# Performance work log

Measured on AMD Instinct MI355X. Metric: run time of the kernel, lower is better.

## Reference

```python
import jax, jax.numpy as jnp
import numpy as np

C, L, B = 66, 100, 4096
FEAT = 9 * C * 12  # 7128


def _conv1d(x, w, b, pad):
    # x: (B, Cin, L), w: (Cout, Cin, K), b: (Cout,)
    y = jax.lax.conv_general_dilated(x, w, (1,), [(pad, pad)],
                                     dimension_numbers=('NCH', 'OIH', 'NCH'))
    return y + b[None, :, None]


def _pool2(x):
    # AvgPool1d(kernel=2, stride=2) with floor on odd lengths
    Lx = x.shape[-1]
    x = x[..., : 2 * (Lx // 2)]
    return x.reshape(*x.shape[:-1], Lx // 2, 2).mean(-1)


def _branch(xc, w1, b1, w2, b2, w3, b3, pad):
    # conv/relu/pool x3 (dropout is identity in eval)
    h = _pool2(jax.nn.relu(_conv1d(xc, w1, b1, pad)))
    h = _pool2(jax.nn.relu(_conv1d(h, w2, b2, pad)))
    h = _pool2(jax.nn.relu(_conv1d(h, w3, b3, pad)))
    return h  # (B, 4, 12)


def setup_inputs() -> dict:
    key = jax.random.key(0)
    ks = jax.random.split(key, 20)
    s = 0.1
    inp = {
        'x': jax.random.normal(ks[0], (B, L, C), dtype=jnp.float32),
        # high-resolution branch (kernel 7, pad 3), one filter set per channel
        'hw1': jax.random.normal(ks[1], (C, 8, 1, 7)) * s,
        'hb1': jnp.full((C, 8), 0.1, jnp.float32),
        'hw2': jax.random.normal(ks[2], (C, 4, 8, 7)) * s,
        'hb2': jnp.full((C, 4), 0.1, jnp.float32),
        'hw3': jax.random.normal(ks[3], (C, 4, 4, 7)) * s,
        'hb3': jnp.full((C, 4), 0.1, jnp.float32),
        # low-resolution branch (kernel 3, pad 1)
        'lw1': jax.random.normal(ks[4], (C, 8, 1, 3)) * s,
        'lb1': jnp.full((C, 8), 0.1, jnp.float32),
        'lw2': jax.random.normal(ks[5], (C, 4, 8, 3)) * s,
        'lb2': jnp.full((C, 4), 0.1, jnp.float32),
        'lw3': jax.random.normal(ks[6], (C, 4, 4, 3)) * s,
        'lb3': jnp.full((C, 4), 0.1, jnp.float32),
        # MLP head
        'fw1': jax.random.normal(ks[7], (1936, FEAT)) * 0.02,
        'fb1': jnp.full((1936,), 0.1, jnp.float32),
        'fw2': jax.random.normal(ks[8], (14, 1936)) * 0.02,
        'fb2': jnp.full((14,), 0.1, jnp.float32),
    }
    return inp


def reference(x, hw1, hb1, hw2, hb2, hw3, hb3,
              lw1, lb1, lw2, lb2, lw3, lb3, fw1, fb1, fw2, fb2):
    bsz = x.shape[0]
    xc = jnp.transpose(x, (2, 0, 1))[:, :, None, :]  # (C, B, 1, L)
    high = jax.vmap(lambda xi, a, b_, c, d, e, f: _branch(xi, a, b_, c, d, e, f, 3))(
        xc, hw1, hb1, hw2, hb2, hw3, hb3)        # (C, B, 4, 12)
    low = jax.vmap(lambda xi, a, b_, c, d, e, f: _branch(xi, a, b_, c, d, e, f, 1))(
        xc, lw1, lb1, lw2, lb2, lw3, lb3)        # (C, B, 4, 12)
    res = jax.vmap(lambda xi: _pool2(_pool2(_pool2(xi))))(xc)  # (C, B, 1, 12)
    feats = jnp.concatenate([high, low, res], axis=2)          # (C, B, 9, 12)
    feats = jnp.transpose(feats, (1, 0, 2, 3)).reshape(bsz, -1)  # (B, C*9*12)
    h = jax.nn.relu(feats @ fw1.T + fb1)
    return h @ fw2.T + fb2
```

## Files before the change

kernel.cpp:

```cpp
#include <hip/hip_runtime.h>

typedef _Float16 f16;
typedef _Float16 h2 __attribute__((ext_vector_type(2)));
typedef _Float16 f16x8 __attribute__((ext_vector_type(8)));
typedef float    f32x4 __attribute__((ext_vector_type(4)));
typedef unsigned int u32;
typedef u32 u32x2 __attribute__((ext_vector_type(2)));
typedef u32 u32x4 __attribute__((ext_vector_type(4)));

#define CCH 66
#define LLEN 100
#define BSZ 4096
#define NPAD 2048
#define NOUT 1936
#define KFEAT 7128
#define FPC 112
#define KF2 (CCH * FPC)
#define KP2 7424
#define NCH2 (KP2 / 8)
#define ROWE (BSZ * 8)
#define LC (LLEN * CCH)
#define OSTR 25
#define XPW 52
#define CWS 512

typedef __attribute__((address_space(1))) const u32 gu32;
typedef __attribute__((address_space(3))) u32 lu32;

__device__ __forceinline__ void gload_lds16(const void* g, void* l) {
    __builtin_amdgcn_global_load_lds((gu32*)g, (lu32*)l, 16, 0, 0);
}

__device__ __forceinline__ h2  uh(u32 v) { return __builtin_bit_cast(h2, v); }
__device__ __forceinline__ u32 hu(h2 v)  { return __builtin_bit_cast(u32, v); }
__device__ __forceinline__ h2  pkfma(h2 a, h2 b, h2 c) { return __builtin_elementwise_fma(a, b, c); }
__device__ __forceinline__ h2  pkmax0(h2 a) { h2 z = (h2)(_Float16)0.f; return __builtin_elementwise_max(a, z); }

__global__ __launch_bounds__(256) void transpose_x(const float* __restrict__ x,
                                                   f16* __restrict__ xT) {
    __shared__ float tile[32][33];
    const int m0 = blockIdx.x * 32;
    const int b0 = blockIdx.y * 32;
    const int tx = threadIdx.x & 31, ty = threadIdx.x >> 5;
#pragma unroll
    for (int i = 0; i < 32; i += 8) {
        int m = m0 + tx, b = b0 + ty + i;
        tile[ty + i][tx] = (m < LC) ? x[(size_t)b * LC + m] : 0.f;
    }
    __syncthreads();
#pragma unroll
    for (int i = 0; i < 32; i += 8) {
        int m = m0 + ty + i, b = b0 + tx;
        if (m < LC) xT[(size_t)m * BSZ + b] = (f16)tile[tx][ty + i];
    }
}

__global__ __launch_bounds__(256) void pack_x(const f16* __restrict__ xT,
                                              u32* __restrict__ xP) {
    const int c = blockIdx.x, w = blockIdx.y;
    const int b = blockIdx.z * 256 + threadIdx.x;
    u32 v = 0u;
    if (w < 50) {
        f16 lo = xT[(size_t)(2 * w * CCH + c) * BSZ + b];
        f16 hi = xT[(size_t)((2 * w + 1) * CCH + c) * BSZ + b];
        v = hu((h2){lo, hi});
    }
    xP[((size_t)c * XPW + w) * BSZ + b] = v;
}

__device__ __forceinline__ u32 dupf(float v) {
    _Float16 h = (_Float16)v; return hu((h2){h, h});
}
__device__ __forceinline__ u32 pk2f(float a, float b) {
    return hu((h2){(_Float16)a, (_Float16)b});
}

__global__ __launch_bounds__(64) void prep_w(
    const float* __restrict__ hw1, const float* __restrict__ hb1,
    const float* __restrict__ hw2, const float* __restrict__ hb2,
    const float* __restrict__ hw3, const float* __restrict__ hb3,
    const float* __restrict__ lw1, const float* __restrict__ lb1,
    const float* __restrict__ lw2, const float* __restrict__ lb2,
    const float* __restrict__ lw3, const float* __restrict__ lb3,
    u32* __restrict__ wpk) {
    const int c = blockIdx.x, t = threadIdx.x;
    u32* wb = wpk + c * CWS;
    for (int i = t; i < 56; i += 64) wb[i] = dupf(hw1[c * 56 + i]);
    if (t < 8)  wb[56 + t] = dupf(hb1[c * 8 + t]);
    for (int i = t; i < 224; i += 64) wb[64 + i] = dupf(hw2[c * 224 + i]);
    if (t < 4)  wb[288 + t] = dupf(hb2[c * 4 + t]);
    for (int i = t; i < 56; i += 64) {
        int pr = i / 28, j = i - pr * 28;
        wb[292 + i] = pk2f(hw3[c * 112 + 2 * pr * 28 + j], hw3[c * 112 + (2 * pr + 1) * 28 + j]);
    }
    if (t < 2)  wb[348 + t] = pk2f(hb3[c * 4 + 2 * t], hb3[c * 4 + 2 * t + 1]);
    for (int i = t; i < 24; i += 64) wb[350 + i] = dupf(lw1[c * 24 + i]);
    if (t < 8)  wb[374 + t] = dupf(lb1[c * 8 + t]);
    for (int i = t; i < 96; i += 64) wb[382 + i] = dupf(lw2[c * 96 + i]);
    if (t < 4)  wb[478 + t] = dupf(lb2[c * 4 + t]);
    for (int i = t; i < 24; i += 64) {
        int pr = i / 12, j = i - pr * 12;
        wb[482 + i] = pk2f(lw3[c * 48 + 2 * pr * 12 + j], lw3[c * 48 + (2 * pr + 1) * 12 + j]);
    }
    if (t < 2)  wb[506 + t] = pk2f(lb3[c * 4 + 2 * t], lb3[c * 4 + 2 * t + 1]);
}

template<int K>
__device__ __forceinline__ void hp1_core(const u32* PX, const u32* __restrict__ w1d,
                                         const u32* __restrict__ b1d, u32 msk, u32 np[8]) {
#pragma unroll
    for (int ic = 0; ic < 8; ++ic) {
        h2 bb = uh(b1d[ic]);
        h2 AL = bb, AH = bb;
#pragma unroll
        for (int k = 0; k < K; ++k) {
            h2 w = uh(w1d[ic * K + k]);
            AL = pkfma(w, uh(PX[k]), AL);
            AH = pkfma(w, uh(PX[k + 2]), AH);
        }
        AL = pkmax0(AL); AH = pkmax0(AH);
        _Float16 cA = (_Float16)0.5f * (AL.x + AL.y);
        _Float16 cB = (_Float16)0.5f * (AH.x + AH.y);
        np[ic] = hu((h2){cA, cB}) & msk;
    }
}

template<int K>
__device__ __forceinline__ void hp1_run(const u32* __restrict__ xlt, int idx,
                                        const u32* w1d, const u32* b1d, u32 np[8]) {
    constexpr int P = K / 2;
    constexpr int NA = (K + 5) / 2;
    const int w0 = idx - (P + 1) / 2;
    const u32* base = xlt + w0 * 256;
    u32 A[NA];
#pragma unroll
    for (int j = 0; j < NA; ++j) A[j] = base[j * 256];
    u32 PX[K + 2];
#pragma unroll
    for (int j = 0; j < K + 2; ++j)
        PX[j] = (j & 1) ? A[(j + 1) / 2]
                        : __builtin_amdgcn_alignbit(A[j / 2 + 1], A[j / 2], 16);
    u32 m = ((idx < 50) ? 0xFFFFu : 0u) | ((idx + 1 < 50) ? 0xFFFF0000u : 0u);
    hp1_core<K>(PX, w1d, b1d, m, np);
}

template<int K, int IDX>
__device__ __forceinline__ void hp1_edge(const u32* __restrict__ xlt,
                                         const u32* w1d, const u32* b1d, u32 np[8]) {
    constexpr int P = K / 2;
    u32 PX[K + 2];
#pragma unroll
    for (int j = 0; j < K + 2; ++j) {
        int u = 2 * IDX - P + j;
        u32 v;
        if (u < -1)      v = 0u;
        else if (u == -1) v = xlt[0] << 16;
        else if (u & 1)  v = __builtin_amdgcn_alignbit(xlt[((u + 1) / 2) * 256],
                                                       xlt[((u - 1) / 2) * 256], 16);
        else             v = xlt[(u / 2) * 256];
        PX[j] = v;
    }
    hp1_core<K>(PX, w1d, b1d, 0xFFFFFFFFu, np);
}

template<int K>
__device__ __forceinline__ void run_branch_pk(const u32* __restrict__ xlt,
                                              const u32* __restrict__ wb,
                                              u32* __restrict__ orow) {
    constexpr int P = K / 2;
    constexpr int NW1 = (K + 1) / 2;
    const u32* w1d = wb;
    const u32* b1d = wb + 8 * K;
    const u32* w2d = b1d + 8;
    const u32* b2d = w2d + 32 * K;
    const u32* w3p = b2d + 4;
    const u32* b3p = w3p + 8 * K;

    u32 W1p[8][NW1];
    u32 W2d[4][K];
#pragma unroll
    for (int ic = 0; ic < 8; ++ic)
#pragma unroll
        for (int j = 0; j < NW1; ++j) W1p[ic][j] = 0u;
#pragma unroll
    for (int oc = 0; oc < 4; ++oc)
#pragma unroll
        for (int k = 0; k < K; ++k) W2d[oc][k] = 0u;

    {
        u32 np[8];
        if (K == 7) {
            hp1_edge<K, 0>(xlt, w1d, b1d, np);
#pragma unroll
            for (int ic = 0; ic < 8; ++ic) W1p[ic][1] = np[ic] << 16;
            hp1_edge<K, 1>(xlt, w1d, b1d, np);
#pragma unroll
            for (int ic = 0; ic < 8; ++ic) W1p[ic][2] = np[ic];
            hp1_edge<K, 3>(xlt, w1d, b1d, np);
#pragma unroll
            for (int ic = 0; ic < 8; ++ic) W1p[ic][3] = np[ic];
        } else {
            hp1_edge<K, 0>(xlt, w1d, b1d, np);
#pragma unroll
            for (int ic = 0; ic < 8; ++ic) W1p[ic][0] = np[ic] << 16;
            hp1_edge<K, 1>(xlt, w1d, b1d, np);
#pragma unroll
            for (int ic = 0; ic < 8; ++ic) W1p[ic][1] = np[ic];
        }
    }

    h2 Pp01 = (h2)(_Float16)0.f, Pp23 = Pp01, Q01 = Pp01, Q23 = Pp01;
    const int SMAX = 23 + P;
    for (int s = 0; s <= SMAX; ++s) {
        h2 Y[4];
#pragma unroll
        for (int oc = 0; oc < 4; ++oc) Y[oc] = uh(b2d[oc]);
#pragma unroll
        for (int ic = 0; ic < 8; ++ic) {
            u32 PW[K];
#pragma unroll
            for (int k = 0; k < K; ++k)
                PW[k] = (k & 1) ? __builtin_amdgcn_alignbit(W1p[ic][k / 2 + 1], W1p[ic][k / 2], 16)
                                : W1p[ic][k / 2];
#pragma unroll
            for (int oc = 0; oc < 4; ++oc)
#pragma unroll
                for (int k = 0; k < K; ++k)
                    Y[oc] = pkfma(uh(w2d[(oc * 8 + ic) * K + k]), uh(PW[k]), Y[oc]);
        }
#pragma unroll
        for (int oc = 0; oc < 4; ++oc) {
            h2 Yr = pkmax0(Y[oc]);
            _Float16 hv = (_Float16)0.5f * (Yr.x + Yr.y);
            u32 d = hu((h2){hv, hv});
            d = (s <= 24) ? d : 0u;
#pragma unroll
            for (int k = 0; k < K - 1; ++k) W2d[oc][k] = W2d[oc][k + 1];
            W2d[oc][K - 1] = d;
        }
        int p = s - P;
        if (p >= 0) {
            h2 Y01 = uh(b3p[0]), Y23 = uh(b3p[1]);
#pragma unroll
            for (int ic = 0; ic < 4; ++ic)
#pragma unroll
                for (int k = 0; k < K; ++k) {
                    h2 wv = uh(W2d[ic][k]);
                    Y01 = pkfma(uh(w3p[ic * K + k]), wv, Y01);
                    Y23 = pkfma(uh(w3p[4 * K + ic * K + k]), wv, Y23);
                }
            Y01 = pkmax0(Y01); Y23 = pkmax0(Y23);
            if ((p & 1) == 0) { Pp01 = Y01; Pp23 = Y23; }
            else {
                h2 hf = (h2)(_Float16)0.5f;
                h2 O01 = (Pp01 + Y01) * hf;
                h2 O23 = (Pp23 + Y23) * hf;
                int t = p >> 1;
                if ((t & 1) == 0) { Q01 = O01; Q23 = O23; }
                else {
                    int w = t >> 1;
                    orow[0 * 6 + w] = hu((h2){Q01.x, O01.x});
                    orow[1 * 6 + w] = hu((h2){Q01.y, O01.y});
                    orow[2 * 6 + w] = hu((h2){Q23.x, O23.x});
                    orow[3 * 6 + w] = hu((h2){Q23.y, O23.y});
                }
            }
        }
        if (s < SMAX) {
            u32 np[8];
            hp1_run<K>(xlt, 2 * s + P + 2, w1d, b1d, np);
#pragma unroll
            for (int ic = 0; ic < 8; ++ic) {
#pragma unroll
                for (int j = 0; j < NW1 - 1; ++j) W1p[ic][j] = W1p[ic][j + 1];
                W1p[ic][NW1 - 1] = np[ic];
            }
        }
    }
}

__global__ __launch_bounds__(256, 2) void feats_kernel(
    const u32* __restrict__ xP, const u32* __restrict__ wpk,
    f16* __restrict__ feats2) {
    __shared__ u32 xl[XPW * 256];
    __shared__ u32 obufw[256 * OSTR];
    const int c = blockIdx.x;
    const int tid = threadIdx.x;
    const int lane = tid & 63, wid = tid >> 6;
    const int b = blockIdx.y * 256 + tid;

    const u32* src = xP + (size_t)c * XPW * BSZ + blockIdx.y * 256;
    for (int w = wid; w < XPW; w += 4)
        gload_lds16(src + (size_t)w * BSZ + lane * 4, (char*)xl + w * 1024 + lane * 16);
    __syncthreads();

    const u32* xlt = xl + tid;
    const u32* wb = wpk + c * CWS;
    u32* orow = obufw + tid * OSTR;
    u32* dst = (u32*)feats2 + (size_t)c * 14 * (ROWE / 2) + (size_t)b * 4;

    run_branch_pk<7>(xlt, wb, orow);
    {
        u32 v[24];
#pragma unroll
        for (int j = 0; j < 24; ++j) v[j] = orow[j];
#pragma unroll
        for (int ch = 0; ch < 6; ++ch)
            *(u32x4*)(dst + (size_t)ch * (ROWE / 2)) =
                (u32x4){v[ch * 4], v[ch * 4 + 1], v[ch * 4 + 2], v[ch * 4 + 3]};
    }
    run_branch_pk<3>(xlt, wb + 350, orow);
    {
        u32 v[24];
#pragma unroll
        for (int j = 0; j < 24; ++j) v[j] = orow[j];
#pragma unroll
        for (int ch = 0; ch < 6; ++ch)
            *(u32x4*)(dst + (size_t)(6 + ch) * (ROWE / 2)) =
                (u32x4){v[ch * 4], v[ch * 4 + 1], v[ch * 4 + 2], v[ch * 4 + 3]};
    }
    u32 orr[6];
#pragma unroll
    for (int t2 = 0; t2 < 6; ++t2) {
        h2 S0 = uh(xlt[(8 * t2 + 0) * 256]) + uh(xlt[(8 * t2 + 1) * 256]) +
                uh(xlt[(8 * t2 + 2) * 256]) + uh(xlt[(8 * t2 + 3) * 256]);
        h2 S1 = uh(xlt[(8 * t2 + 4) * 256]) + uh(xlt[(8 * t2 + 5) * 256]) +
                uh(xlt[(8 * t2 + 6) * 256]) + uh(xlt[(8 * t2 + 7) * 256]);
        _Float16 o0 = (_Float16)0.125f * (S0.x + S0.y);
        _Float16 o1 = (_Float16)0.125f * (S1.x + S1.y);
        orr[t2] = hu((h2){o0, o1});
    }
    *(u32x4*)(dst + (size_t)12 * (ROWE / 2)) = (u32x4){orr[0], orr[1], orr[2], orr[3]};
    *(u32x4*)(dst + (size_t)13 * (ROWE / 2)) = (u32x4){orr[4], orr[5], 0u, 0u};
}

__global__ void zero_pad2(f16* __restrict__ feats2) {
    int idx = blockIdx.x * 256 + threadIdx.x;
    u32* dst = (u32*)(feats2 + (size_t)(CCH * 14) * ROWE);
    if (idx < (4 * ROWE * 2) / 16)
        *(u32x4*)(dst + idx * 4) = (u32x4){0u, 0u, 0u, 0u};
}

__global__ void cvt_fw1(const float* __restrict__ fw1, f16* __restrict__ dst) {
    int n = blockIdx.y;
    int kp = blockIdx.x * 256 + threadIdx.x;
    if (kp >= KP2) return;
    int c2 = kp / FPC, f = kp - c2 * FPC;
    float v = 0.f;
    if (n < NOUT && kp < KF2 && f < 108)
        v = fw1[(size_t)n * KFEAT + c2 * 108 + f];
    dst[(size_t)n * KP2 + kp] = (f16)v;
}

__global__ __launch_bounds__(256) void fc1_gemm(
    const f16* __restrict__ A, const f16* __restrict__ Bw, float* __restrict__ C) {
    __shared__ f16 lds_a[128 * 32];
    __shared__ f16 lds_b[128 * 32];
    const int tid = threadIdx.x;
    const int bm = blockIdx.x, bn = blockIdx.y, kz = blockIdx.z;
    const int wid = tid >> 6, lane = tid & 63;
    const int wm = wid >> 1, wn = wid & 1;

    f32x4 acc[4][4];
#pragma unroll
    for (int i = 0; i < 4; ++i)
#pragma unroll
        for (int j = 0; j < 4; ++j) acc[i][j] = (f32x4){0.f, 0.f, 0.f, 0.f};

    const f16* Bbase = Bw + (size_t)bn * 128 * KP2;
    const int l15 = lane & 15, lhi = lane >> 4;

    const int flat0 = tid, flat1 = 256 + tid;
    const int row0 = flat0 >> 2, kc0 = flat0 & 3;
    const int row1 = flat1 >> 2, kc1 = flat1 & 3;

    const int kbeg = kz * (KP2 / 2), kend = kbeg + KP2 / 2;
    for (int k0 = kbeg; k0 < kend; k0 += 32) {
        __syncthreads();
        gload_lds16(A + (size_t)((k0 >> 3) + kc0) * ROWE + (size_t)(bm * 128 + row0) * 8,
                    (char*)lds_a + flat0 * 16);
        gload_lds16(A + (size_t)((k0 >> 3) + kc1) * ROWE + (size_t)(bm * 128 + row1) * 8,
                    (char*)lds_a + flat1 * 16);
        gload_lds16(Bbase + (size_t)row0 * KP2 + k0 + kc0 * 8, (char*)lds_b + flat0 * 16);
        gload_lds16(Bbase + (size_t)row1 * KP2 + k0 + kc1 * 8, (char*)lds_b + flat1 * 16);
        __syncthreads();

        f16x8 af[4], bf[4];
#pragma unroll
        for (int i = 0; i < 4; ++i) {
            int m = wm * 64 + i * 16 + l15;
            af[i] = *(const f16x8*)(lds_a + m * 32 + lhi * 8);
            int n = wn * 64 + i * 16 + l15;
            bf[i] = *(const f16x8*)(lds_b + n * 32 + lhi * 8);
        }
#pragma unroll
        for (int i = 0; i < 4; ++i)
#pragma unroll
            for (int j = 0; j < 4; ++j)
                acc[i][j] = __builtin_amdgcn_mfma_f32_16x16x32_f16(af[i], bf[j], acc[i][j], 0, 0, 0);
    }

#pragma unroll
    for (int i = 0; i < 4; ++i)
#pragma unroll
        for (int j = 0; j < 4; ++j) {
            int n = bn * 128 + wn * 64 + j * 16 + l15;
#pragma unroll
            for (int r = 0; r < 4; ++r) {
                int m = bm * 128 + wm * 64 + i * 16 + lhi * 4 + r;
                atomicAdd(&C[(size_t)m * NPAD + n], acc[i][j][r]);
            }
        }
}

__global__ __launch_bounds__(256) void fc1_fin(const float* __restrict__ C,
                                               const float* __restrict__ fb1,
                                               f16* __restrict__ H) {
    size_t i4 = ((size_t)blockIdx.x * 256 + threadIdx.x) * 4;
    int n = (int)(i4 & (NPAD - 1));
    f32x4 v = *(const f32x4*)(C + i4);
    f16 r[4];
#pragma unroll
    for (int j = 0; j < 4; ++j) {
        int nn = n + j;
        float bias = (nn < NOUT) ? fb1[nn] : 0.f;
        r[j] = (f16)fmaxf(v[j] + bias, 0.f);
    }
    *(u32x2*)(H + i4) = (u32x2){hu((h2){r[0], r[1]}), hu((h2){r[2], r[3]})};
}

__global__ __launch_bounds__(64) void fc2_kernel(const f16* __restrict__ H,
                                                 const float* __restrict__ fw2,
                                                 const float* __restrict__ fb2,
                                                 float* __restrict__ out) {
    const int b = blockIdx.x;
    const int t = threadIdx.x;
    const f16* hb = H + (size_t)b * NPAD;
    float acc[14];
#pragma unroll
    for (int o = 0; o < 14; ++o) acc[o] = 0.f;
    for (int k = t; k < NOUT; k += 64) {
        float hv = (float)hb[k];
#pragma unroll
        for (int o = 0; o < 14; ++o) acc[o] += hv * fw2[o * NOUT + k];
    }
#pragma unroll
    for (int o = 0; o < 14; ++o) {
        float v = acc[o];
#pragma unroll
        for (int off = 32; off > 0; off >>= 1) v += __shfl_down(v, off, 64);
        if (t == 0) out[b * 14 + o] = v + fb2[o];
    }
}

extern "C" void kernel_launch(void* const* d_in, const int* in_sizes, int n_in,
                              void* d_out, int out_size, void* d_ws, size_t ws_size,
                              hipStream_t stream) {
    const float* x   = (const float*)d_in[0];
    const float* hw1 = (const float*)d_in[1];
    const float* hb1 = (const float*)d_in[2];
    const float* hw2 = (const float*)d_in[3];
    const float* hb2 = (const float*)d_in[4];
    const float* hw3 = (const float*)d_in[5];
    const float* hb3 = (const float*)d_in[6];
    const float* lw1 = (const float*)d_in[7];
    const float* lb1 = (const float*)d_in[8];
    const float* lw2 = (const float*)d_in[9];
    const float* lb2 = (const float*)d_in[10];
    const float* lw3 = (const float*)d_in[11];
    const float* lb3 = (const float*)d_in[12];
    const float* fw1 = (const float*)d_in[13];
    const float* fb1 = (const float*)d_in[14];
    const float* fw2 = (const float*)d_in[15];
    const float* fb2 = (const float*)d_in[16];

    char* wsb = (char*)d_ws;
    f16*  feats2 = (f16*)wsb;
    char* reg2   = wsb + (size_t)NCH2 * ROWE * 2;
    f16*  xT     = (f16*)reg2;
    float* C     = (float*)reg2;
    f16*  h      = (f16*)(reg2 + (size_t)BSZ * NPAD * 4);
    char* reg3   = reg2 + (size_t)LC * BSZ * 2;
    u32*  xP     = (u32*)reg3;
    f16*  fw1H   = (f16*)reg3;
    u32*  wpk    = (u32*)(reg3 + (size_t)CCH * XPW * BSZ * 4);

    transpose_x<<<dim3((LC + 31) / 32, BSZ / 32), 256, 0, stream>>>(x, xT);
    pack_x<<<dim3(CCH, XPW, BSZ / 256), 256, 0, stream>>>(xT, xP);
    prep_w<<<dim3(CCH), 64, 0, stream>>>(hw1, hb1, hw2, hb2, hw3, hb3,
                                         lw1, lb1, lw2, lb2, lw3, lb3, wpk);
    feats_kernel<<<dim3(CCH, BSZ / 256), 256, 0, stream>>>(xP, wpk, feats2);
    zero_pad2<<<dim3(64), 256, 0, stream>>>(feats2);
    cvt_fw1<<<dim3((KP2 + 255) / 256, NPAD), 256, 0, stream>>>(fw1, fw1H);
    hipMemsetAsync(C, 0, (size_t)BSZ * NPAD * 4, stream);
    fc1_gemm<<<dim3(BSZ / 128, NPAD / 128, 2), 256, 0, stream>>>(feats2, fw1H, C);
    fc1_fin<<<dim3(BSZ * NPAD / 4 / 256), 256, 0, stream>>>(C, fb1, h);
    fc2_kernel<<<dim3(BSZ), 64, 0, stream>>>(h, fw2, fb2, (float*)d_out);
}
```

Before: 783.2 us.

## Fuse transpose and pack of x, stream input windows from global in feats kernel

Replaces the two-pass transpose_x plus pack_x pipeline with a single xpose_pack kernel that reads x tiles into LDS and writes the packed half2 layout directly, plus a small kernel that zeroes the halo words. The feats kernel drops its large LDS staging buffer and instead keeps a sliding register window of input pairs, loaded from global memory as the convolution advances. This removes an intermediate f16 buffer round trip and frees LDS, which may allow more occupancy. The cost is more global loads in the inner loop, which rely on cache hits and latency hiding.

After: 757.1 us. 3.3% less time.

```diff
diff --git a/kernel.cpp b/kernel.cpp
--- a/kernel.cpp
+++ b/kernel.cpp
@@ -36,36 +36,31 @@
 __device__ __forceinline__ h2  pkfma(h2 a, h2 b, h2 c) { return __builtin_elementwise_fma(a, b, c); }
 __device__ __forceinline__ h2  pkmax0(h2 a) { h2 z = (h2)(_Float16)0.f; return __builtin_elementwise_max(a, z); }
 
-__global__ __launch_bounds__(256) void transpose_x(const float* __restrict__ x,
-                                                   f16* __restrict__ xT) {
-    __shared__ float tile[32][33];
-    const int m0 = blockIdx.x * 32;
-    const int b0 = blockIdx.y * 32;
-    const int tx = threadIdx.x & 31, ty = threadIdx.x >> 5;
-#pragma unroll
-    for (int i = 0; i < 32; i += 8) {
-        int m = m0 + tx, b = b0 + ty + i;
-        tile[ty + i][tx] = (m < LC) ? x[(size_t)b * LC + m] : 0.f;
+__global__ __launch_bounds__(256) void xpose_pack(const float* __restrict__ x,
+                                                  u32* __restrict__ xP) {
+    __shared__ float tile[64][133];
+    const int w = blockIdx.x;
+    const int b0 = blockIdx.y * 64;
+    const int tid = threadIdx.x;
+    const float* src = x + (size_t)b0 * LC + (size_t)(2 * w) * CCH;
+#pragma unroll
+    for (int i = 0; i < 33; ++i) {
+        int f = i * 256 + tid;
+        int bi = f / 132, j = f - bi * 132;
+        tile[bi][j] = src[(size_t)bi * LC + j];
     }
     __syncthreads();
-#pragma unroll
-    for (int i = 0; i < 32; i += 8) {
-        int m = m0 + ty + i, b = b0 + tx;
-        if (m < LC) xT[(size_t)m * BSZ + b] = (f16)tile[tx][ty + i];
-    }
-}
-
-__global__ __launch_bounds__(256) void pack_x(const f16* __restrict__ xT,
-                                              u32* __restrict__ xP) {
-    const int c = blockIdx.x, w = blockIdx.y;
-    const int b = blockIdx.z * 256 + threadIdx.x;
-    u32 v = 0u;
-    if (w < 50) {
-        f16 lo = xT[(size_t)(2 * w * CCH + c) * BSZ + b];
-        f16 hi = xT[(size_t)((2 * w + 1) * CCH + c) * BSZ + b];
-        v = hu((h2){lo, hi});
-    }
-    xP[((size_t)c * XPW + w) * BSZ + b] = v;
+    const int lane = tid & 63, cg = tid >> 6;
+    for (int c = cg; c < CCH; c += 4) {
+        u32 v = hu((h2){(_Float16)tile[lane][c], (_Float16)tile[lane][66 + c]});
+        xP[((size_t)c * XPW + w) * BSZ + b0 + lane] = v;
+    }
+}
+
+__global__ __launch_bounds__(256) void zero_halo_xp(u32* __restrict__ xP) {
+    const int c = blockIdx.x;
+    const int i = blockIdx.y * 256 + threadIdx.x;
+    *(u32x4*)(xP + ((size_t)c * XPW + 50) * BSZ + (size_t)i * 4) = (u32x4){0u, 0u, 0u, 0u};
 }
 
 __device__ __forceinline__ u32 dupf(float v) {
@@ -125,16 +120,9 @@
     }
 }
 
-template<int K>
-__device__ __forceinline__ void hp1_run(const u32* __restrict__ xlt, int idx,
+template<int K, int NA>
+__device__ __forceinline__ void hp1_win(const u32 A[NA], int idx,
                                         const u32* w1d, const u32* b1d, u32 np[8]) {
-    constexpr int P = K / 2;
-    constexpr int NA = (K + 5) / 2;
-    const int w0 = idx - (P + 1) / 2;
-    const u32* base = xlt + w0 * 256;
-    u32 A[NA];
-#pragma unroll
-    for (int j = 0; j < NA; ++j) A[j] = base[j * 256];
     u32 PX[K + 2];
 #pragma unroll
     for (int j = 0; j < K + 2; ++j)
@@ -145,7 +133,7 @@
 }
 
 template<int K, int IDX>
-__device__ __forceinline__ void hp1_edge(const u32* __restrict__ xlt,
+__device__ __forceinline__ void hp1_edge(const u32* __restrict__ xg,
                                          const u32* w1d, const u32* b1d, u32 np[8]) {
     constexpr int P = K / 2;
     u32 PX[K + 2];
@@ -154,21 +142,23 @@
         int u = 2 * IDX - P + j;
         u32 v;
         if (u < -1)      v = 0u;
-        else if (u == -1) v = xlt[0] << 16;
-        else if (u & 1)  v = __builtin_amdgcn_alignbit(xlt[((u + 1) / 2) * 256],
-                                                       xlt[((u - 1) / 2) * 256], 16);
-        else             v = xlt[(u / 2) * 256];
+        else if (u == -1) v = xg[0] << 16;
+        else if (u & 1)  v = __builtin_amdgcn_alignbit(xg[(size_t)((u + 1) / 2) * BSZ],
+                                                       xg[(size_t)((u - 1) / 2) * BSZ], 16);
+        else             v = xg[(size_t)(u / 2) * BSZ];
         PX[j] = v;
     }
     hp1_core<K>(PX, w1d, b1d, 0xFFFFFFFFu, np);
 }
 
 template<int K>
-__device__ __forceinline__ void run_branch_pk(const u32* __restrict__ xlt,
+__device__ __forceinline__ void run_branch_pk(const u32* __restrict__ xg,
                                               const u32* __restrict__ wb,
                                               u32* __restrict__ orow) {
     constexpr int P = K / 2;
     constexpr int NW1 = (K + 1) / 2;
+    constexpr int NA = (K == 7) ? 6 : 4;
+    constexpr int WB = (K == 7) ? 3 : 2;
     const u32* w1d = wb;
     const u32* b1d = wb + 8 * K;
     const u32* w2d = b1d + 8;
@@ -190,24 +180,28 @@
     {
         u32 np[8];
         if (K == 7) {
-            hp1_edge<K, 0>(xlt, w1d, b1d, np);
+            hp1_edge<K, 0>(xg, w1d, b1d, np);
 #pragma unroll
             for (int ic = 0; ic < 8; ++ic) W1p[ic][1] = np[ic] << 16;
-            hp1_edge<K, 1>(xlt, w1d, b1d, np);
+            hp1_edge<K, 1>(xg, w1d, b1d, np);
 #pragma unroll
             for (int ic = 0; ic < 8; ++ic) W1p[ic][2] = np[ic];
-            hp1_edge<K, 3>(xlt, w1d, b1d, np);
+            hp1_edge<K, 3>(xg, w1d, b1d, np);
 #pragma unroll
             for (int ic = 0; ic < 8; ++ic) W1p[ic][3] = np[ic];
         } else {
-            hp1_edge<K, 0>(xlt, w1d, b1d, np);
+            hp1_edge<K, 0>(xg, w1d, b1d, np);
 #pragma unroll
             for (int ic = 0; ic < 8; ++ic) W1p[ic][0] = np[ic] << 16;
-            hp1_edge<K, 1>(xlt, w1d, b1d, np);
+            hp1_edge<K, 1>(xg, w1d, b1d, np);
 #pragma unroll
             for (int ic = 0; ic < 8; ++ic) W1p[ic][1] = np[ic];
         }
     }
+
+    u32 XA[NA];
+#pragma unroll
+    for (int j = 0; j < NA; ++j) XA[j] = xg[(size_t)(WB + j) * BSZ];
 
     h2 Pp01 = (h2)(_Float16)0.f, Pp23 = Pp01, Q01 = Pp01, Q23 = Pp01;
     const int SMAX = 23 + P;
@@ -268,13 +262,17 @@
         }
         if (s < SMAX) {
             u32 np[8];
-            hp1_run<K>(xlt, 2 * s + P + 2, w1d, b1d, np);
+            hp1_win<K, NA>(XA, 2 * s + P + 2, w1d, b1d, np);
 #pragma unroll
             for (int ic = 0; ic < 8; ++ic) {
 #pragma unroll
                 for (int j = 0; j < NW1 - 1; ++j) W1p[ic][j] = W1p[ic][j + 1];
                 W1p[ic][NW1 - 1] = np[ic];
             }
+#pragma unroll
+            for (int j = 0; j < NA - 2; ++j) XA[j] = XA[j + 2];
+            XA[NA - 2] = xg[(size_t)(WB + 2 * s + NA) * BSZ];
+            XA[NA - 1] = xg[(size_t)(WB + 2 * s + NA + 1) * BSZ];
         }
     }
 }
@@ -282,24 +280,17 @@
 __global__ __launch_bounds__(256, 2) void feats_kernel(
     const u32* __restrict__ xP, const u32* __restrict__ wpk,
     f16* __restrict__ feats2) {
-    __shared__ u32 xl[XPW * 256];
     __shared__ u32 obufw[256 * OSTR];
     const int c = blockIdx.x;
     const int tid = threadIdx.x;
-    const int lane = tid & 63, wid = tid >> 6;
     const int b = blockIdx.y * 256 + tid;
 
-    const u32* src = xP + (size_t)c * XPW * BSZ + blockIdx.y * 256;
-    for (int w = wid; w < XPW; w += 4)
-        gload_lds16(src + (size_t)w * BSZ + lane * 4, (char*)xl + w * 1024 + lane * 16);
-    __syncthreads();
-
-    const u32* xlt = xl + tid;
+    const u32* xg = xP + (size_t)c * XPW * BSZ + b;
     const u32* wb = wpk + c * CWS;
     u32* orow = obufw + tid * OSTR;
     u32* dst = (u32*)feats2 + (size_t)c * 14 * (ROWE / 2) + (size_t)b * 4;
 
-    run_branch_pk<7>(xlt, wb, orow);
+    run_branch_pk<7>(xg, wb, orow);
     {
         u32 v[24];
 #pragma unroll
@@ -309,7 +300,7 @@
             *(u32x4*)(dst + (size_t)ch * (ROWE / 2)) =
                 (u32x4){v[ch * 4], v[ch * 4 + 1], v[ch * 4 + 2], v[ch * 4 + 3]};
     }
-    run_branch_pk<3>(xlt, wb + 350, orow);
+    run_branch_pk<3>(xg, wb + 350, orow);
     {
         u32 v[24];
 #pragma unroll
@@ -322,10 +313,10 @@
     u32 orr[6];
 #pragma unroll
     for (int t2 = 0; t2 < 6; ++t2) {
-        h2 S0 = uh(xlt[(8 * t2 + 0) * 256]) + uh(xlt[(8 * t2 + 1) * 256]) +
-                uh(xlt[(8 * t2 + 2) * 256]) + uh(xlt[(8 * t2 + 3) * 256]);
-        h2 S1 = uh(xlt[(8 * t2 + 4) * 256]) + uh(xlt[(8 * t2 + 5) * 256]) +
-                uh(xlt[(8 * t2 + 6) * 256]) + uh(xlt[(8 * t2 + 7) * 256]);
+        h2 S0 = uh(xg[(size_t)(8 * t2 + 0) * BSZ]) + uh(xg[(size_t)(8 * t2 + 1) * BSZ]) +
+                uh(xg[(size_t)(8 * t2 + 2) * BSZ]) + uh(xg[(size_t)(8 * t2 + 3) * BSZ]);
+        h2 S1 = uh(xg[(size_t)(8 * t2 + 4) * BSZ]) + uh(xg[(size_t)(8 * t2 + 5) * BSZ]) +
+                uh(xg[(size_t)(8 * t2 + 6) * BSZ]) + uh(xg[(size_t)(8 * t2 + 7) * BSZ]);
         _Float16 o0 = (_Float16)0.125f * (S0.x + S0.y);
         _Float16 o1 = (_Float16)0.125f * (S1.x + S1.y);
         orr[t2] = hu((h2){o0, o1});
@@ -477,16 +468,15 @@
     char* wsb = (char*)d_ws;
     f16*  feats2 = (f16*)wsb;
     char* reg2   = wsb + (size_t)NCH2 * ROWE * 2;
-    f16*  xT     = (f16*)reg2;
     float* C     = (float*)reg2;
     f16*  h      = (f16*)(reg2 + (size_t)BSZ * NPAD * 4);
-    char* reg3   = reg2 + (size_t)LC * BSZ * 2;
+    char* reg3   = reg2 + 54067200;
     u32*  xP     = (u32*)reg3;
     f16*  fw1H   = (f16*)reg3;
     u32*  wpk    = (u32*)(reg3 + (size_t)CCH * XPW * BSZ * 4);
 
-    transpose_x<<<dim3((LC + 31) / 32, BSZ / 32), 256, 0, stream>>>(x, xT);
-    pack_x<<<dim3(CCH, XPW, BSZ / 256), 256, 0, stream>>>(xT, xP);
+    xpose_pack<<<dim3(50, BSZ / 64), 256, 0, stream>>>(x, xP);
+    zero_halo_xp<<<dim3(CCH, 8), 256, 0, stream>>>(xP);
     prep_w<<<dim3(CCH), 64, 0, stream>>>(hw1, hb1, hw2, hb2, hw3, hb3,
                                          lw1, lb1, lw2, lb2, lw3, lb3, wpk);
     feats_kernel<<<dim3(CCH, BSZ / 256), 256, 0, stream>>>(xP, wpk, feats2);
```
